# Optimization experiments

Measured on AMD Instinct MI355X. Metric: run time of the kernel, lower is better.

The kernel has to match this reference:

```python
import jax, jax.numpy as jnp
import numpy as np

EMBED_DIM = 1024
NUM_HEADS = 16
HEAD_DIM = EMBED_DIM // NUM_HEADS


def setup_inputs() -> dict:
    key = jax.random.key(0)
    k_x, k_wqkv, k_bqkv, k_wo, k_bo = jax.random.split(key, 5)
    B, T, C = 4, 2048, EMBED_DIM
    bound = 1.0 / np.sqrt(C)
    return {
        "x": jax.random.normal(k_x, (B, T, C), dtype=jnp.float32),
        "w_qkv": jax.random.uniform(k_wqkv, (C, 3 * C), jnp.float32, -bound, bound),
        "b_qkv": jax.random.uniform(k_bqkv, (3 * C,), jnp.float32, -bound, bound),
        "w_out": jax.random.uniform(k_wo, (C, C), jnp.float32, -bound, bound),
        "b_out": jax.random.uniform(k_bo, (C,), jnp.float32, -bound, bound),
    }


def reference(x, w_qkv, b_qkv, w_out, b_out):
    B, T, C = x.shape
    H, D = NUM_HEADS, HEAD_DIM
    qkv = x @ w_qkv + b_qkv                       # [B,T,3C]
    qkv = qkv.reshape(B, T, 3, H, D)
    q, k, v = qkv[:, :, 0], qkv[:, :, 1], qkv[:, :, 2]  # [B,T,H,D]
    scale = 1.0 / np.sqrt(D).astype(np.float32)
    scores = jnp.einsum("bqhd,bkhd->bhqk", q, k) * scale  # [B,H,T,T]
    causal = jnp.tril(jnp.ones((T, T), dtype=bool))
    scores = jnp.where(causal, scores, -jnp.inf)
    attn = jax.nn.softmax(scores, axis=-1)
    # dropout p=0.0 / eval mode -> identity
    ctx = jnp.einsum("bhqk,bkhd->bqhd", attn, v).reshape(B, T, C)
    return ctx @ w_out + b_out
```

## Files before the change

kernel.cpp:

```cpp
#include <hip/hip_runtime.h>
#include <hip/hip_bf16.h>

#define NB 4
#define NT 2048
#define NC 1024
#define NH 16
#define ND 64
#define BT (NB*NT)
#define LOG2E 1.4426950408889634f
#define NEG_BIG (-3.0e38f)
#define MLC 28.853900817779268f

typedef __attribute__((ext_vector_type(8))) short bf16x8;
typedef __attribute__((ext_vector_type(4))) float f32x4;

static __device__ __forceinline__ short f2bf(float f) {
    union { float f; unsigned u; } v; v.f = f;
    unsigned r = (v.u + 0x7fffu + ((v.u >> 16) & 1u)) >> 16;
    return (short)r;
}

static __device__ __forceinline__ unsigned pk2(float a, float b) {
#if __has_builtin(__builtin_amdgcn_cvt_pk_bf16_f32)
    auto v = __builtin_amdgcn_cvt_pk_bf16_f32(a, b);
    union { decltype(v) v; unsigned u; } c; c.v = v; return c.u;
#else
    return (unsigned)(unsigned short)f2bf(a) | ((unsigned)(unsigned short)f2bf(b) << 16);
#endif
}

static __device__ __forceinline__ f32x4 mfma16(bf16x8 a, bf16x8 b, f32x4 c) {
    return __builtin_amdgcn_mfma_f32_16x16x32_bf16(a, b, c, 0, 0, 0);
}

static __device__ __forceinline__ float fexp2(float x) {
#if __has_builtin(__builtin_amdgcn_exp2f)
    return __builtin_amdgcn_exp2f(x);
#else
    return exp2f(x);
#endif
}

template<int GOFF>
static __device__ __forceinline__ void gload_lds16(const short* g, short* l) {
    __builtin_amdgcn_global_load_lds(
        (const __attribute__((address_space(1))) void*)g,
        (__attribute__((address_space(3))) void*)l,
        16, GOFF, 0);
}

__global__ __launch_bounds__(256)
void xcvt(const float* __restrict__ x, short* __restrict__ xb)
{
    const size_t i = ((size_t)blockIdx.x * 256 + threadIdx.x) * 8;
    float4 f0 = *(const float4*)(x + i);
    float4 f1 = *(const float4*)(x + i + 4);
    uint4 p;
    p.x = pk2(f0.x, f0.y); p.y = pk2(f0.z, f0.w);
    p.z = pk2(f1.x, f1.y); p.w = pk2(f1.z, f1.w);
    *(uint4*)(xb + i) = p;
}

__global__ __launch_bounds__(256)
void transpose_w(const float* __restrict__ w, short* __restrict__ wt, int R, int Cn)
{
    __shared__ short t[64][72];
    const int tid = threadIdx.x;
    const int r0 = blockIdx.x * 64;
    const int c0 = blockIdx.y * 64;
    {
        const int rl = tid >> 2, c4 = (tid & 3) << 4;
        const float* src = w + (size_t)(r0 + rl) * Cn + c0 + c4;
        float4 f0 = *(const float4*)(src + 0);
        float4 f1 = *(const float4*)(src + 4);
        float4 f2 = *(const float4*)(src + 8);
        float4 f3 = *(const float4*)(src + 12);
        short* d = &t[rl][c4];
        d[0]=f2bf(f0.x); d[1]=f2bf(f0.y); d[2]=f2bf(f0.z); d[3]=f2bf(f0.w);
        d[4]=f2bf(f1.x); d[5]=f2bf(f1.y); d[6]=f2bf(f1.z); d[7]=f2bf(f1.w);
        d[8]=f2bf(f2.x); d[9]=f2bf(f2.y); d[10]=f2bf(f2.z); d[11]=f2bf(f2.w);
        d[12]=f2bf(f3.x); d[13]=f2bf(f3.y); d[14]=f2bf(f3.z); d[15]=f2bf(f3.w);
    }
    __syncthreads();
    {
        const int cl = tid >> 2, r4 = (tid & 3) << 4;
        bf16x8 p0, p1;
#pragma unroll
        for (int j = 0; j < 8; ++j) { p0[j] = t[r4 + j][cl]; p1[j] = t[r4 + 8 + j][cl]; }
        short* dst = wt + (size_t)(c0 + cl) * R + r0 + r4;
        *(bf16x8*)dst       = p0;
        *(bf16x8*)(dst + 8) = p1;
    }
}

__global__ __launch_bounds__(512, 2)
void qkv_gemm8(const short* __restrict__ xb, const short* __restrict__ wt,
               const float* __restrict__ bias,
               short* __restrict__ q, short* __restrict__ k, short* __restrict__ vt)
{
    __shared__ short aLds[3][256 * 64];
    __shared__ short bLds[3][128 * 64];
    const int tid  = threadIdx.x;
    const int lane = tid & 63;
    const int wave = tid >> 6;
    const int waveM = wave & 1;
    const int waveN = wave >> 1;
    const int quad = lane >> 4;
    const int l15  = lane & 15;
    const int l7   = l15 & 7;
    const int m0 = blockIdx.x * 256;
    const int n0 = blockIdx.y * 128;

    const int rsub = lane >> 3;
    const int gcol = ((lane & 7) ^ rsub) * 8;

    f32x4 acc[8][2];
#pragma unroll
    for (int i = 0; i < 8; ++i)
#pragma unroll
        for (int j = 0; j < 2; ++j) acc[i][j] = 0.0f;

    bf16x8 aF[4][2];
    bf16x8 bF[2][2];

    auto stA = [&](int bufi, int kt) {
#pragma unroll
        for (int c = 0; c < 4; ++c) {
            const int rb = c*64 + wave*8;
            gload_lds16<0>(xb + (size_t)(m0 + rb + rsub) * NC + kt*64 + gcol,
                           &aLds[bufi][rb * 64]);
        }
    };
    auto stB = [&](int bufi, int kt) {
#pragma unroll
        for (int c = 0; c < 2; ++c) {
            const int rb = c*64 + wave*8;
            gload_lds16<0>(wt + (size_t)(n0 + rb + rsub) * NC + kt*64 + gcol,
                           &bLds[bufi][rb * 64]);
        }
    };
    auto rdA = [&](int bufi, int mh) {
#pragma unroll
        for (int mi = 0; mi < 4; ++mi)
#pragma unroll
            for (int kd = 0; kd < 2; ++kd) {
                const int r = waveM*128 + mh*64 + mi*16 + l15;
                aF[mi][kd] = *(const bf16x8*)
                    &aLds[bufi][r*64 + (((kd*4 + quad) ^ l7) * 8)];
            }
    };
    auto rdB = [&](int bufi) {
#pragma unroll
        for (int ni = 0; ni < 2; ++ni)
#pragma unroll
            for (int kd = 0; kd < 2; ++kd) {
                const int r = waveN*32 + ni*16 + l15;
                bF[ni][kd] = *(const bf16x8*)
                    &bLds[bufi][r*64 + (((kd*4 + quad) ^ l7) * 8)];
            }
    };
    auto mmQ = [&](int mh) {
        __builtin_amdgcn_s_setprio(1);
#pragma unroll
        for (int mi = 0; mi < 4; ++mi)
#pragma unroll
            for (int ni = 0; ni < 2; ++ni) {
                f32x4 c = acc[mh*4 + mi][ni];
                c = mfma16(aF[mi][0], bF[ni][0], c);
                c = mfma16(aF[mi][1], bF[ni][1], c);
                acc[mh*4 + mi][ni] = c;
            }
        __builtin_amdgcn_s_setprio(0);
    };

    stA(0, 0); stB(0, 0);
    stA(1, 1); stB(1, 1);
    asm volatile("s_waitcnt vmcnt(6)" ::: "memory");
    __builtin_amdgcn_s_barrier();

    int cur = 0;
#pragma unroll 1
    for (int kt = 0; kt < 16; ++kt) {
        const int stg = (cur >= 1) ? cur - 1 : 2;
        rdA(cur, 0); rdB(cur);
        if (kt + 2 < 16) stA(stg, kt + 2);
        asm volatile("s_waitcnt lgkmcnt(8)" ::: "memory");
        __builtin_amdgcn_s_barrier();
        asm volatile("s_waitcnt lgkmcnt(0)" ::: "memory");
        mmQ(0);
        __builtin_amdgcn_s_barrier();
        rdA(cur, 1);
        if (kt + 2 < 16) stB(stg, kt + 2);
        __builtin_amdgcn_s_barrier();
        asm volatile("s_waitcnt lgkmcnt(0)" ::: "memory");
        mmQ(1);
        if (kt + 2 < 16)      asm volatile("s_waitcnt vmcnt(6)" ::: "memory");
        else if (kt + 1 < 16) asm volatile("s_waitcnt vmcnt(0)" ::: "memory");
        __builtin_amdgcn_s_barrier();
        cur = (cur == 2) ? 0 : cur + 1;
    }

#pragma unroll
    for (int mi = 0; mi < 8; ++mi) {
#pragma unroll
        for (int ni = 0; ni < 2; ++ni) {
            const int n = n0 + waveN*32 + ni*16 + l15;
            const float bb = bias[n];
            const int s = n >> 10;
            const int h = (n >> 6) & 15;
            const int d = n & 63;
#pragma unroll
            for (int r = 0; r < 4; ++r) {
                const int m = m0 + waveM*128 + mi*16 + quad*4 + r;
                const int b = m >> 11;
                const int t = m & (NT - 1);
                const float val = acc[mi][ni][r] + bb;
                const size_t bhx = (size_t)(b * NH + h);
                if (s == 0)      q [(bhx * NT + t) * ND + d] = f2bf(val * 0.125f);
                else if (s == 1) k [(bhx * NT + t) * ND + d] = f2bf(val);
                else             vt[(bhx * ND + d) * NT + t] = f2bf(val);
            }
        }
    }
}

__global__ __launch_bounds__(256)
void attn(const short* __restrict__ q, const short* __restrict__ k,
          const short* __restrict__ vt, short* __restrict__ ctx)
{
    __shared__ short kbuf[2][64 * 64];
    __shared__ short vbuf[2][64 * 64];
    __shared__ short pbuf[4][32 * 64];
    const int tid  = threadIdx.x;
    const int lane = tid & 63;
    const int wave = tid >> 6;
    const int quad = lane >> 4;
    const int l15  = lane & 15;
    const int l7   = l15 & 7;
    const int bh = blockIdx.x;
    const int b  = bh >> 4;
    const int h  = bh & 15;

    const short* Qp = q  + (size_t)bh * NT * ND;
    const short* Kp = k  + (size_t)bh * NT * ND;
    const short* Vp = vt + (size_t)bh * ND * NT;

    const int srow   = lane >> 3;
    const int schunk = ((lane & 7) ^ srow) * 8;
    short* pw = &pbuf[wave][0];

    for (int half = 0; half < 2; ++half) {
        const int qblock = half ? (15 - (int)blockIdx.y) : (int)blockIdx.y;
        const int qb  = qblock * 128;
        const int wq0 = qb + wave * 32;
        const int ktB = 2 * qblock + 2;

        bf16x8 qf[2][2];
#pragma unroll
        for (int mi = 0; mi < 2; ++mi)
#pragma unroll
            for (int kd = 0; kd < 2; ++kd)
                qf[mi][kd] = *(const bf16x8*)(Qp + (size_t)(wq0 + mi*16 + l15) * ND + kd*32 + quad*8);

        f32x4 ot[4][2];
        f32x4 lv[2];
#pragma unroll
        for (int di = 0; di < 4; ++di)
#pragma unroll
            for (int mi = 0; mi < 2; ++mi) ot[di][mi] = 0.0f;
        lv[0] = 0.0f; lv[1] = 0.0f;

        {
            const short* Ks = Kp + (size_t)(wave*16 + srow) * ND + schunk;
            gload_lds16<0>(Ks,          &kbuf[0][(wave*16    ) * 64]);
            gload_lds16<0>(Ks + 8*ND,   &kbuf[0][(wave*16 + 8) * 64]);
            const short* Vs = Vp + (size_t)(wave*16 + srow) * NT + schunk;
            gload_lds16<0>(Vs,          &vbuf[0][(wave*16    ) * 64]);
            gload_lds16<0>(Vs + 8*NT,   &vbuf[0][(wave*16 + 8) * 64]);
        }

        for (int kt = 0; kt < ktB; ++kt) {
            const int p  = kt & 1;
            const int kb = kt << 6;
            __syncthreads();

            if (kt + 1 < ktB) {
                const int kb2 = kb + 64;
                const short* Ks = Kp + (size_t)(kb2 + wave*16 + srow) * ND + schunk;
                gload_lds16<0>(Ks,        &kbuf[1-p][(wave*16    ) * 64]);
                gload_lds16<0>(Ks + 8*ND, &kbuf[1-p][(wave*16 + 8) * 64]);
                const short* Vs = Vp + (size_t)(wave*16 + srow) * NT + kb2 + schunk;
                gload_lds16<0>(Vs,        &vbuf[1-p][(wave*16    ) * 64]);
                gload_lds16<0>(Vs + 8*NT, &vbuf[1-p][(wave*16 + 8) * 64]);
            }

            if (kb > wq0 + 31) continue;

            bf16x8 kf[4][2];
#pragma unroll
            for (int ni = 0; ni < 4; ++ni)
#pragma unroll
                for (int kd = 0; kd < 2; ++kd)
                    kf[ni][kd] = *(const bf16x8*)
                        &kbuf[p][(ni*16 + l15)*64 + (((kd*4 + quad) ^ l7) * 8)];

            f32x4 st[4][2];
#pragma unroll
            for (int ni = 0; ni < 4; ++ni)
#pragma unroll
                for (int mi = 0; mi < 2; ++mi) {
                    st[ni][mi] = 0.0f;
                    st[ni][mi] = mfma16(kf[ni][0], qf[mi][0], st[ni][mi]);
                    st[ni][mi] = mfma16(kf[ni][1], qf[mi][1], st[ni][mi]);
                }

            if (kb + 63 > wq0) {
#pragma unroll
                for (int ni = 0; ni < 4; ++ni)
#pragma unroll
                    for (int mi = 0; mi < 2; ++mi) {
                        const int qrow = wq0 + mi*16 + l15;
#pragma unroll
                        for (int r = 0; r < 4; ++r) {
                            const int key = kb + ni*16 + quad*4 + r;
                            if (key > qrow) st[ni][mi][r] = NEG_BIG;
                        }
                    }
            }

#pragma unroll
            for (int mi = 0; mi < 2; ++mi) {
#pragma unroll
                for (int ni = 0; ni < 4; ++ni) {
#pragma unroll
                    for (int r = 0; r < 4; ++r)
                        st[ni][mi][r] = fexp2(fmaf(st[ni][mi][r], LOG2E, -MLC));
                    lv[mi] += st[ni][mi];
                    const f32x4 v = st[ni][mi];
                    *(uint2*)&pw[(mi*16 + l15)*64
                                 + (((2*ni + (quad >> 1)) ^ l7) * 8)
                                 + (quad & 1) * 4] =
                        make_uint2(pk2(v[0], v[1]), pk2(v[2], v[3]));
                }
            }

            bf16x8 vf[4][2], pf[2][2];
#pragma unroll
            for (int di = 0; di < 4; ++di)
#pragma unroll
                for (int kd = 0; kd < 2; ++kd)
                    vf[di][kd] = *(const bf16x8*)
                        &vbuf[p][(di*16 + l15)*64 + (((kd*4 + quad) ^ l7) * 8)];
#pragma unroll
            for (int mi = 0; mi < 2; ++mi)
#pragma unroll
                for (int kd = 0; kd < 2; ++kd)
                    pf[mi][kd] = *(const bf16x8*)
                        &pw[(mi*16 + l15)*64 + (((kd*4 + quad) ^ l7) * 8)];

#pragma unroll
            for (int di = 0; di < 4; ++di)
#pragma unroll
                for (int mi = 0; mi < 2; ++mi) {
                    ot[di][mi] = mfma16(vf[di][0], pf[mi][0], ot[di][mi]);
                    ot[di][mi] = mfma16(vf[di][1], pf[mi][1], ot[di][mi]);
                }
        }

#pragma unroll
        for (int mi = 0; mi < 2; ++mi) {
            float l = lv[mi][0] + lv[mi][1] + lv[mi][2] + lv[mi][3];
            l += __shfl_xor(l, 16);
            l += __shfl_xor(l, 32);
            const float inv = 1.0f / l;
            const int t = wq0 + mi*16 + l15;
            short* dst = ctx + ((size_t)(b * NT + t)) * NC + h*64 + quad*4;
#pragma unroll
            for (int di = 0; di < 4; ++di) {
                const f32x4 v = ot[di][mi] * inv;
                *(uint2*)(dst + di*16) = make_uint2(pk2(v[0], v[1]), pk2(v[2], v[3]));
            }
        }
        __syncthreads();
    }
}

__global__ __launch_bounds__(256)
void out_gemm(const short* __restrict__ a, const short* __restrict__ wt,
              const float* __restrict__ bias, float* __restrict__ out)
{
    __shared__ short aLds[128 * 64];
    __shared__ short bLds[128 * 64];
    const int tid  = threadIdx.x;
    const int lane = tid & 63;
    const int wave = tid >> 6;
    const int waveM = wave & 1;
    const int waveN = wave >> 1;
    const int quad = lane >> 4;
    const int l15  = lane & 15;
    const int l7   = l15 & 7;
    const int m0 = blockIdx.x * 128;
    const int n0 = blockIdx.y * 128;

    const int rsub   = lane >> 3;
    const int cchunk = (lane & 7) ^ rsub;
    const int gcol   = cchunk * 8;

    f32x4 acc[4][4];
#pragma unroll
    for (int i = 0; i < 4; ++i)
#pragma unroll
        for (int j = 0; j < 4; ++j) acc[i][j] = 0.0f;

    for (int k0 = 0; k0 < NC; k0 += 64) {
#pragma unroll
        for (int i = 0; i < 4; ++i) {
            const int rbase = wave * 32 + i * 8;
            gload_lds16<0>(a + (size_t)(m0 + rbase + rsub) * NC + k0 + gcol,
                           &aLds[rbase * 64]);
        }
#pragma unroll
        for (int i = 0; i < 4; ++i) {
            const int rbase = wave * 32 + i * 8;
            gload_lds16<0>(wt + (size_t)(n0 + rbase + rsub) * NC + k0 + gcol,
                           &bLds[rbase * 64]);
        }
        __syncthreads();

#pragma unroll
        for (int kd = 0; kd < 2; ++kd) {
            bf16x8 af[4], bfr[4];
#pragma unroll
            for (int mi = 0; mi < 4; ++mi) {
                const int r = waveM*64 + mi*16 + l15;
                af[mi] = *(const bf16x8*)&aLds[r*64 + (((kd*4 + quad) ^ l7) * 8)];
            }
#pragma unroll
            for (int ni = 0; ni < 4; ++ni) {
                const int r = waveN*64 + ni*16 + l15;
                bfr[ni] = *(const bf16x8*)&bLds[r*64 + (((kd*4 + quad) ^ l7) * 8)];
            }
#pragma unroll
            for (int mi = 0; mi < 4; ++mi)
#pragma unroll
                for (int ni = 0; ni < 4; ++ni)
                    acc[mi][ni] = mfma16(af[mi], bfr[ni], acc[mi][ni]);
        }
        __syncthreads();
    }

#pragma unroll
    for (int mi = 0; mi < 4; ++mi) {
#pragma unroll
        for (int ni = 0; ni < 4; ++ni) {
            const int n = n0 + waveN*64 + ni*16 + l15;
            const float bb = bias[n];
#pragma unroll
            for (int r = 0; r < 4; ++r) {
                const int m = m0 + waveM*64 + mi*16 + quad*4 + r;
                out[(size_t)m * NC + n] = acc[mi][ni][r] + bb;
            }
        }
    }
}

extern "C" void kernel_launch(void* const* d_in, const int* in_sizes, int n_in,
                              void* d_out, int out_size, void* d_ws, size_t ws_size,
                              hipStream_t stream)
{
    const float* x     = (const float*)d_in[0];
    const float* w_qkv = (const float*)d_in[1];
    const float* b_qkv = (const float*)d_in[2];
    const float* w_out = (const float*)d_in[3];
    const float* b_out = (const float*)d_in[4];
    float* out = (float*)d_out;

    const size_t SZ = (size_t)NB * NH * NT * ND;
    short* q   = (short*)d_ws;
    short* kk  = q  + SZ;
    short* vt  = kk + SZ;
    short* ctx = vt + SZ;
    short* xbf = ctx + SZ;
    short* wTq = ctx;
    short* wTo = xbf;

    hipLaunchKernelGGL(xcvt, dim3(BT*NC/(256*8)), dim3(256), 0, stream, x, xbf);
    hipLaunchKernelGGL(transpose_w, dim3(16, 48), dim3(256), 0, stream,
                       w_qkv, wTq, NC, 3*NC);
    hipLaunchKernelGGL(qkv_gemm8, dim3(BT/256, (3*NC)/128), dim3(512), 0, stream,
                       xbf, wTq, b_qkv, q, kk, vt);
    hipLaunchKernelGGL(attn, dim3(NB*NH, 8), dim3(256), 0, stream,
                       q, kk, vt, ctx);
    hipLaunchKernelGGL(transpose_w, dim3(16, 16), dim3(256), 0, stream,
                       w_out, wTo, NC, NC);
    hipLaunchKernelGGL(out_gemm, dim3(BT/128, NC/128), dim3(256), 0, stream,
                       ctx, wTo, b_out, out);
}
```

Before: 273.4 us.

## Port out-projection GEMM to 8-wave triple-buffered pipeline and remap QKV wave tiling

Replaces the simple single-buffered 128x128 out-projection GEMM with a 512-thread, 256x128-tile kernel using a three-stage LDS pipeline of async global-to-LDS loads and split B-fragment MFMA phases, copied from the QKV GEMM. The QKV GEMM's wave layout also changes from 2x4 to 4x2, so each wave covers a 64x64 sub-tile and its A fragments are reused across two B halves instead of reloading A. The aim is to overlap memory loads with MFMA work and reduce LDS fragment traffic. The out GEMM now launches only 256 blocks, which may leave part of the GPU idle.

```diff
diff --git a/kernel.cpp b/kernel.cpp
--- a/kernel.cpp
+++ b/kernel.cpp
@@ -103,8 +103,8 @@
     const int tid  = threadIdx.x;
     const int lane = tid & 63;
     const int wave = tid >> 6;
-    const int waveM = wave & 1;
-    const int waveN = wave >> 1;
+    const int waveM = wave & 3;
+    const int waveN = wave >> 2;
     const int quad = lane >> 4;
     const int l15  = lane & 15;
     const int l7   = l15 & 7;
@@ -114,11 +114,11 @@
     const int rsub = lane >> 3;
     const int gcol = ((lane & 7) ^ rsub) * 8;
 
-    f32x4 acc[8][2];
-#pragma unroll
-    for (int i = 0; i < 8; ++i)
-#pragma unroll
-        for (int j = 0; j < 2; ++j) acc[i][j] = 0.0f;
+    f32x4 acc[4][4];
+#pragma unroll
+    for (int i = 0; i < 4; ++i)
+#pragma unroll
+        for (int j = 0; j < 4; ++j) acc[i][j] = 0.0f;
 
     bf16x8 aF[4][2];
     bf16x8 bF[2][2];
@@ -139,36 +139,36 @@
                            &bLds[bufi][rb * 64]);
         }
     };
-    auto rdA = [&](int bufi, int mh) {
+    auto rdA = [&](int bufi) {
 #pragma unroll
         for (int mi = 0; mi < 4; ++mi)
 #pragma unroll
             for (int kd = 0; kd < 2; ++kd) {
-                const int r = waveM*128 + mh*64 + mi*16 + l15;
+                const int r = waveM*64 + mi*16 + l15;
                 aF[mi][kd] = *(const bf16x8*)
                     &aLds[bufi][r*64 + (((kd*4 + quad) ^ l7) * 8)];
             }
     };
-    auto rdB = [&](int bufi) {
+    auto rdB = [&](int bufi, int nh) {
 #pragma unroll
         for (int ni = 0; ni < 2; ++ni)
 #pragma unroll
             for (int kd = 0; kd < 2; ++kd) {
-                const int r = waveN*32 + ni*16 + l15;
+                const int r = waveN*64 + nh*32 + ni*16 + l15;
                 bF[ni][kd] = *(const bf16x8*)
                     &bLds[bufi][r*64 + (((kd*4 + quad) ^ l7) * 8)];
             }
     };
-    auto mmQ = [&](int mh) {
+    auto mmQ = [&](int nh) {
         __builtin_amdgcn_s_setprio(1);
 #pragma unroll
         for (int mi = 0; mi < 4; ++mi)
 #pragma unroll
             for (int ni = 0; ni < 2; ++ni) {
-                f32x4 c = acc[mh*4 + mi][ni];
+                f32x4 c = acc[mi][nh*2 + ni];
                 c = mfma16(aF[mi][0], bF[ni][0], c);
                 c = mfma16(aF[mi][1], bF[ni][1], c);
-                acc[mh*4 + mi][ni] = c;
+                acc[mi][nh*2 + ni] = c;
             }
         __builtin_amdgcn_s_setprio(0);
     };
@@ -182,14 +182,14 @@
 #pragma unroll 1
     for (int kt = 0; kt < 16; ++kt) {
         const int stg = (cur >= 1) ? cur - 1 : 2;
-        rdA(cur, 0); rdB(cur);
+        rdA(cur); rdB(cur, 0);
         if (kt + 2 < 16) stA(stg, kt + 2);
         asm volatile("s_waitcnt lgkmcnt(8)" ::: "memory");
         __builtin_amdgcn_s_barrier();
         asm volatile("s_waitcnt lgkmcnt(0)" ::: "memory");
         mmQ(0);
         __builtin_amdgcn_s_barrier();
-        rdA(cur, 1);
+        rdB(cur, 1);
         if (kt + 2 < 16) stB(stg, kt + 2);
         __builtin_amdgcn_s_barrier();
         asm volatile("s_waitcnt lgkmcnt(0)" ::: "memory");
@@ -201,20 +201,20 @@
     }
 
 #pragma unroll
-    for (int mi = 0; mi < 8; ++mi) {
-#pragma unroll
-        for (int ni = 0; ni < 2; ++ni) {
-            const int n = n0 + waveN*32 + ni*16 + l15;
+    for (int mi = 0; mi < 4; ++mi) {
+#pragma unroll
+        for (int nj = 0; nj < 4; ++nj) {
+            const int n = n0 + waveN*64 + nj*16 + l15;
             const float bb = bias[n];
             const int s = n >> 10;
             const int h = (n >> 6) & 15;
             const int d = n & 63;
 #pragma unroll
             for (int r = 0; r < 4; ++r) {
-                const int m = m0 + waveM*128 + mi*16 + quad*4 + r;
+                const int m = m0 + waveM*64 + mi*16 + quad*4 + r;
                 const int b = m >> 11;
                 const int t = m & (NT - 1);
-                const float val = acc[mi][ni][r] + bb;
+                const float val = acc[mi][nj][r] + bb;
                 const size_t bhx = (size_t)(b * NH + h);
                 if (s == 0)      q [(bhx * NT + t) * ND + d] = f2bf(val * 0.125f);
                 else if (s == 1) k [(bhx * NT + t) * ND + d] = f2bf(val);
@@ -385,26 +385,25 @@
     }
 }
 
-__global__ __launch_bounds__(256)
-void out_gemm(const short* __restrict__ a, const short* __restrict__ wt,
-              const float* __restrict__ bias, float* __restrict__ out)
+__global__ __launch_bounds__(512, 2)
+void out_gemm8(const short* __restrict__ a, const short* __restrict__ wt,
+               const float* __restrict__ bias, float* __restrict__ out)
 {
-    __shared__ short aLds[128 * 64];
-    __shared__ short bLds[128 * 64];
+    __shared__ short aLds[3][256 * 64];
+    __shared__ short bLds[3][128 * 64];
     const int tid  = threadIdx.x;
     const int lane = tid & 63;
     const int wave = tid >> 6;
-    const int waveM = wave & 1;
-    const int waveN = wave >> 1;
+    const int waveM = wave & 3;
+    const int waveN = wave >> 2;
     const int quad = lane >> 4;
     const int l15  = lane & 15;
     const int l7   = l15 & 7;
-    const int m0 = blockIdx.x * 128;
+    const int m0 = blockIdx.x * 256;
     const int n0 = blockIdx.y * 128;
 
-    const int rsub   = lane >> 3;
-    const int cchunk = (lane & 7) ^ rsub;
-    const int gcol   = cchunk * 8;
+    const int rsub = lane >> 3;
+    const int gcol = ((lane & 7) ^ rsub) * 8;
 
     f32x4 acc[4][4];
 #pragma unroll
@@ -412,53 +411,96 @@
 #pragma unroll
         for (int j = 0; j < 4; ++j) acc[i][j] = 0.0f;
 
-    for (int k0 = 0; k0 < NC; k0 += 64) {
-#pragma unroll
-        for (int i = 0; i < 4; ++i) {
-            const int rbase = wave * 32 + i * 8;
-            gload_lds16<0>(a + (size_t)(m0 + rbase + rsub) * NC + k0 + gcol,
-                           &aLds[rbase * 64]);
-        }
-#pragma unroll
-        for (int i = 0; i < 4; ++i) {
-            const int rbase = wave * 32 + i * 8;
-            gload_lds16<0>(wt + (size_t)(n0 + rbase + rsub) * NC + k0 + gcol,
-                           &bLds[rbase * 64]);
-        }
-        __syncthreads();
-
-#pragma unroll
-        for (int kd = 0; kd < 2; ++kd) {
-            bf16x8 af[4], bfr[4];
-#pragma unroll
-            for (int mi = 0; mi < 4; ++mi) {
+    bf16x8 aF[4][2];
+    bf16x8 bF[2][2];
+
+    auto stA = [&](int bufi, int kt) {
+#pragma unroll
+        for (int c = 0; c < 4; ++c) {
+            const int rb = c*64 + wave*8;
+            gload_lds16<0>(a + (size_t)(m0 + rb + rsub) * NC + kt*64 + gcol,
+                           &aLds[bufi][rb * 64]);
+        }
+    };
+    auto stB = [&](int bufi, int kt) {
+#pragma unroll
+        for (int c = 0; c < 2; ++c) {
+            const int rb = c*64 + wave*8;
+            gload_lds16<0>(wt + (size_t)(n0 + rb + rsub) * NC + kt*64 + gcol,
+                           &bLds[bufi][rb * 64]);
+        }
+    };
+    auto rdA = [&](int bufi) {
+#pragma unroll
+        for (int mi = 0; mi < 4; ++mi)
+#pragma unroll
+            for (int kd = 0; kd < 2; ++kd) {
                 const int r = waveM*64 + mi*16 + l15;
-                af[mi] = *(const bf16x8*)&aLds[r*64 + (((kd*4 + quad) ^ l7) * 8)];
-            }
-#pragma unroll
-            for (int ni = 0; ni < 4; ++ni) {
-                const int r = waveN*64 + ni*16 + l15;
-                bfr[ni] = *(const bf16x8*)&bLds[r*64 + (((kd*4 + quad) ^ l7) * 8)];
-            }
-#pragma unroll
-            for (int mi = 0; mi < 4; ++mi)
-#pragma unroll
-                for (int ni = 0; ni < 4; ++ni)
-                    acc[mi][ni] = mfma16(af[mi], bfr[ni], acc[mi][ni]);
-        }
-        __syncthreads();
+                aF[mi][kd] = *(const bf16x8*)
+                    &aLds[bufi][r*64 + (((kd*4 + quad) ^ l7) * 8)];
+            }
+    };
+    auto rdB = [&](int bufi, int nh) {
+#pragma unroll
+        for (int ni = 0; ni < 2; ++ni)
+#pragma unroll
+            for (int kd = 0; kd < 2; ++kd) {
+                const int r = waveN*64 + nh*32 + ni*16 + l15;
+                bF[ni][kd] = *(const bf16x8*)
+                    &bLds[bufi][r*64 + (((kd*4 + quad) ^ l7) * 8)];
+            }
+    };
+    auto mmQ = [&](int nh) {
+        __builtin_amdgcn_s_setprio(1);
+#pragma unroll
+        for (int mi = 0; mi < 4; ++mi)
+#pragma unroll
+            for (int ni = 0; ni < 2; ++ni) {
+                f32x4 c = acc[mi][nh*2 + ni];
+                c = mfma16(aF[mi][0], bF[ni][0], c);
+                c = mfma16(aF[mi][1], bF[ni][1], c);
+                acc[mi][nh*2 + ni] = c;
+            }
+        __builtin_amdgcn_s_setprio(0);
+    };
+
+    stA(0, 0); stB(0, 0);
+    stA(1, 1); stB(1, 1);
+    asm volatile("s_waitcnt vmcnt(6)" ::: "memory");
+    __builtin_amdgcn_s_barrier();
+
+    int cur = 0;
+#pragma unroll 1
+    for (int kt = 0; kt < 16; ++kt) {
+        const int stg = (cur >= 1) ? cur - 1 : 2;
+        rdA(cur); rdB(cur, 0);
+        if (kt + 2 < 16) stA(stg, kt + 2);
+        asm volatile("s_waitcnt lgkmcnt(8)" ::: "memory");
+        __builtin_amdgcn_s_barrier();
+        asm volatile("s_waitcnt lgkmcnt(0)" ::: "memory");
+        mmQ(0);
+        __builtin_amdgcn_s_barrier();
+        rdB(cur, 1);
+        if (kt + 2 < 16) stB(stg, kt + 2);
+        __builtin_amdgcn_s_barrier();
+        asm volatile("s_waitcnt lgkmcnt(0)" ::: "memory");
+        mmQ(1);
+        if (kt + 2 < 16)      asm volatile("s_waitcnt vmcnt(6)" ::: "memory");
+        else if (kt + 1 < 16) asm volatile("s_waitcnt vmcnt(0)" ::: "memory");
+        __builtin_amdgcn_s_barrier();
+        cur = (cur == 2) ? 0 : cur + 1;
     }
 
 #pragma unroll
     for (int mi = 0; mi < 4; ++mi) {
 #pragma unroll
-        for (int ni = 0; ni < 4; ++ni) {
-            const int n = n0 + waveN*64 + ni*16 + l15;
+        for (int nj = 0; nj < 4; ++nj) {
+            const int n = n0 + waveN*64 + nj*16 + l15;
             const float bb = bias[n];
 #pragma unroll
             for (int r = 0; r < 4; ++r) {
                 const int m = m0 + waveM*64 + mi*16 + quad*4 + r;
-                out[(size_t)m * NC + n] = acc[mi][ni][r] + bb;
+                out[(size_t)m * NC + n] = acc[mi][nj][r] + bb;
             }
         }
     }
@@ -493,6 +535,6 @@
                        q, kk, vt, ctx);
     hipLaunchKernelGGL(transpose_w, dim3(16, 16), dim3(256), 0, stream,
                        w_out, wTo, NC, NC);
-    hipLaunchKernelGGL(out_gemm, dim3(BT/128, NC/128), dim3(256), 0, stream,
+    hipLaunchKernelGGL(out_gemm8, dim3(BT/256, NC/128), dim3(512), 0, stream,
                        ctx, wTo, b_out, out);
 }
```

Result: faster. 266.0 us (-2.7%).
